# Kernel optimization log

Hardware: AMD Instinct MI355X
Metric: run time of the kernel (lower is better)

Reference implementation:

```python
import jax, jax.numpy as jnp
import numpy as np

N, I, O, ITERS = 65536, 16, 16, 3
EPS = 1e-8


def hamilton(q, r):
    # Hamilton quaternion product, broadcasting over leading dims; q, r: [..., 4]
    w1, x1, y1, z1 = jnp.moveaxis(q, -1, 0)
    w2, x2, y2, z2 = jnp.moveaxis(r, -1, 0)
    return jnp.stack([
        w1 * w2 - x1 * x2 - y1 * y2 - z1 * z2,
        w1 * x2 + x1 * w2 + y1 * z2 - z1 * y2,
        w1 * y2 - x1 * z2 + y1 * w2 + z1 * x2,
        w1 * z2 + x1 * y2 - y1 * x2 + z1 * w2,
    ], axis=-1)


def squash(s):
    # capsule squash nonlinearity along the last (quaternion) axis
    n2 = jnp.sum(s * s, axis=-1, keepdims=True)
    return s * (n2 / (1.0 + n2)) / jnp.sqrt(n2 + EPS)


def setup_inputs() -> dict:
    key = jax.random.key(0)
    ks = jax.random.split(key, 7)
    return {
        "x": jax.random.normal(ks[0], (N, I, 4), dtype=jnp.float32),
        "quats": jax.random.normal(ks[1], (O, I, 4), dtype=jnp.float32),
        "scale": jax.random.normal(ks[2], (O, I, 1), dtype=jnp.float32),
        "trans": jax.random.normal(ks[3], (O, I, 3), dtype=jnp.float32),
        "bias": jax.random.normal(ks[4], (O,), dtype=jnp.float32),
        "beta": jax.random.normal(ks[5], (O,), dtype=jnp.float32),
        "alpha": jax.random.normal(ks[6], (O,), dtype=jnp.float32),
    }


def reference(x, quats, scale, trans, bias, beta, alpha):
    # normalize learned quaternions to unit rotations: [O, I, 4]
    qn = quats / jnp.sqrt(jnp.sum(quats * quats, axis=-1, keepdims=True) + EPS)
    # votes: rotate each input capsule pose by each (out,in) quaternion -> [N, O, I, 4]
    votes = scale[None] * hamilton(qn[None], x[:, None])
    # translate the vector (imaginary) part of the vote quaternion
    votes = jnp.concatenate([votes[..., :1], votes[..., 1:] + trans[None]], axis=-1)

    b = jnp.zeros((x.shape[0], O, I), dtype=x.dtype)  # routing logits
    for _ in range(ITERS):
        c = jax.nn.softmax(b, axis=1)                    # couple over output caps
        s = jnp.einsum('noi,noid->nod', c, votes)        # weighted vote sum [N,O,4]
        v = squash(s)                                    # output poses [N,O,4]
        b = b + jnp.einsum('nod,noid->noi', v, votes)    # agreement update

    norm_s = jnp.sqrt(jnp.sum(s * s, axis=-1) + EPS)     # [N, O]
    a = jax.nn.sigmoid(beta * norm_s + alpha + bias)     # output activations [N, O]
    return v * a[..., None]                              # activation-scaled poses [N,O,4]
```

## Files before the change

### kernel.cpp

```cpp
#include <hip/hip_runtime.h>
#include <math.h>

#define EPSQ 1e-8f
#define LOG2E 1.4426950408889634f

typedef float f2 __attribute__((ext_vector_type(2)));

__device__ __forceinline__ float rcp_fast(float x) { return __builtin_amdgcn_rcpf(x); }
__device__ __forceinline__ float rsq_fast(float x) { return __builtin_amdgcn_rsqf(x); }
__device__ __forceinline__ f2 pk_fma(f2 a, f2 b, f2 c) { return __builtin_elementwise_fma(a, b, c); }

#define DPP_F(x, ctrl) \
    __int_as_float(__builtin_amdgcn_update_dpp(0, __float_as_int(x), (ctrl), 0xF, 0xF, true))

__device__ __forceinline__ float allsum16(float v) {
    v += DPP_F(v, 0xB1);
    v += DPP_F(v, 0x4E);
    v += DPP_F(v, 0x124);
    v += DPP_F(v, 0x128);
    return v;
}

__global__ __launch_bounds__(256, 4) void caps_kernel(
    const float* __restrict__ x,
    const float* __restrict__ quats,
    const float* __restrict__ scale,
    const float* __restrict__ trans,
    const float* __restrict__ bias,
    const float* __restrict__ beta,
    const float* __restrict__ alpha,
    float* __restrict__ out)
{
    __shared__ __align__(16) float qs[16][16][4];
    __shared__ __align__(16) float tr[16][16][4];
    __shared__ __align__(16) float xs[16][68];

    const int tid = threadIdx.x;
    const int o   = tid & 15;
    const int ln  = tid >> 4;

    {
        const int o2 = tid & 15, i2 = tid >> 4;
        const int pidx = o2 * 16 + i2;
        const float4 q = ((const float4*)quats)[pidx];
        const float sc = scale[pidx];
        const float qn2 = q.x*q.x + q.y*q.y + q.z*q.z + q.w*q.w;
        const float f = sc * rsq_fast(qn2 + EPSQ);
        qs[i2][o2][0] = q.x * f;
        qs[i2][o2][1] = q.y * f;
        qs[i2][o2][2] = q.z * f;
        qs[i2][o2][3] = q.w * f;
        tr[i2][o2][0] = 0.0f;
        tr[i2][o2][1] = trans[pidx*3 + 0];
        tr[i2][o2][2] = trans[pidx*3 + 1];
        tr[i2][o2][3] = trans[pidx*3 + 2];
    }
    {
        const float4 xv = ((const float4*)x)[(size_t)blockIdx.x * 256 + tid];
        *(float4*)&xs[tid >> 4][(tid & 15) * 4] = xv;
    }
    __syncthreads();

    f2 vwx[16], vyz[16];
    #pragma unroll
    for (int i = 0; i < 16; ++i) {
        const float4 q4 = *(const float4*)&qs[i][o][0];
        const float4 t4 = *(const float4*)&tr[i][o][0];
        const float4 x4 = *(const float4*)&xs[ln][i * 4];
        f2 a, b2;
        a = pk_fma(f2{ q4.x,  q4.x}, f2{x4.x, x4.y}, f2{t4.x, t4.y});
        a = pk_fma(f2{-q4.y,  q4.y}, f2{x4.y, x4.x}, a);
        a = pk_fma(f2{-q4.z,  q4.z}, f2{x4.z, x4.w}, a);
        a = pk_fma(f2{-q4.w, -q4.w}, f2{x4.w, x4.z}, a);
        b2 = pk_fma(f2{ q4.x,  q4.x}, f2{x4.z, x4.w}, f2{t4.z, t4.w});
        b2 = pk_fma(f2{-q4.y,  q4.y}, f2{x4.w, x4.z}, b2);
        b2 = pk_fma(f2{ q4.z, -q4.z}, f2{x4.x, x4.y}, b2);
        b2 = pk_fma(f2{ q4.w,  q4.w}, f2{x4.y, x4.x}, b2);
        vwx[i] = a; vyz[i] = b2;
    }

    f2 vl01, vl23;
    f2 v001, v023;
    f2 s01, s23, v01, v23;

    {
        f2 u01 = f2{0.f, 0.f}, u23 = f2{0.f, 0.f};
        #pragma unroll
        for (int i = 0; i < 16; ++i) { u01 += vwx[i]; u23 += vyz[i]; }
        f2 d = u01 * u01;
        d = pk_fma(u23, u23, d);
        const float n2 = (d.x + d.y) * (1.0f / 256.0f);
        const float f = n2 * rcp_fast(1.f + n2) * rsq_fast(n2 + EPSQ) * 0.0625f;
        v001 = u01 * f; v023 = u23 * f;
        vl01 = v001 * LOG2E; vl23 = v023 * LOG2E;
    }

    #pragma unroll
    for (int it = 1; it < 3; ++it) {
        f2 sn01 = f2{0.f, 0.f}, sn23 = f2{0.f, 0.f};
        #pragma unroll
        for (int i = 0; i < 16; ++i) {
            f2 d = vl01 * vwx[i];
            d = pk_fma(vl23, vyz[i], d);
            const float e  = __builtin_amdgcn_exp2f(d.x + d.y);
            const float se = allsum16(e);
            const float c  = e * rcp_fast(se);
            sn01 = pk_fma(f2{c, c}, vwx[i], sn01);
            sn23 = pk_fma(f2{c, c}, vyz[i], sn23);
        }
        s01 = sn01; s23 = sn23;
        const float n2 = s01.x*s01.x + s01.y*s01.y + s23.x*s23.x + s23.y*s23.y;
        const float f = n2 * rcp_fast(1.f + n2) * rsq_fast(n2 + EPSQ);
        v01 = s01 * f; v23 = s23 * f;
        if (it == 1) {
            vl01 = (v001 + v01) * LOG2E;
            vl23 = (v023 + v23) * LOG2E;
        }
    }

    const float n2f = s01.x*s01.x + s01.y*s01.y + s23.x*s23.x + s23.y*s23.y;
    const float norm_s = sqrtf(n2f + EPSQ);
    const float tgt = beta[o] * norm_s + alpha[o] + bias[o];
    const float a = rcp_fast(1.f + __builtin_amdgcn_exp2f(-tgt * LOG2E));
    float4 ov;
    ov.x = v01.x * a; ov.y = v01.y * a; ov.z = v23.x * a; ov.w = v23.y * a;
    ((float4*)out)[(size_t)blockIdx.x * 256 + tid] = ov;
}

extern "C" void kernel_launch(void* const* d_in, const int* in_sizes, int n_in,
                              void* d_out, int out_size, void* d_ws, size_t ws_size,
                              hipStream_t stream) {
    const float* x     = (const float*)d_in[0];
    const float* quats = (const float*)d_in[1];
    const float* scale = (const float*)d_in[2];
    const float* trans = (const float*)d_in[3];
    const float* bias  = (const float*)d_in[4];
    const float* beta  = (const float*)d_in[5];
    const float* alpha = (const float*)d_in[6];
    float* out = (float*)d_out;

    const int N = in_sizes[0] / 64;
    dim3 grid(N / 16), block(256);
    caps_kernel<<<grid, block, 0, stream>>>(x, quats, scale, trans, bias, beta, alpha, out);
}
```

Before: 97.56 us.

## Split input-capsule dimension across lanes and precompute weight table in setup kernel

Each thread now handles four input capsules instead of sixteen, with the per-sample reduction over inputs done via cross-row shuffles, and the grid grows to four samples per block. Quaternion normalization and sign-arranged coefficients are precomputed once by a separate one-block setup kernel into workspace, so the main kernel's prologue is plain copies. This aims to cut registers per thread and increase parallelism, at the cost of four times more blocks, redundant table loads per block, extra shuffle reductions, an extra launch, and only a quarter of lanes writing output.

```diff
diff --git a/kernel.cpp b/kernel.cpp
--- a/kernel.cpp
+++ b/kernel.cpp
@@ -20,111 +20,134 @@
     v += DPP_F(v, 0x128);
     return v;
 }
+__device__ __forceinline__ float allsum_rows(float v) {
+    v += __shfl_xor(v, 16);
+    v += __shfl_xor(v, 32);
+    return v;
+}
+
+__global__ void setup_kernel(const float* __restrict__ quats,
+                             const float* __restrict__ scale,
+                             const float* __restrict__ trans,
+                             float4* __restrict__ ws) {
+    const int t = threadIdx.x;
+    const int k = t >> 6, l = t & 63;
+    const int r = l >> 4, o = l & 15;
+    const int i = 4 * k + r;
+    const int pidx = o * 16 + i;
+    const float4 q = ((const float4*)quats)[pidx];
+    const float sc = scale[pidx];
+    const float f = sc * rsq_fast(q.x*q.x + q.y*q.y + q.z*q.z + q.w*q.w + EPSQ);
+    const float w = q.x * f, x = q.y * f, y = q.z * f, z = q.w * f;
+    ws[t]       = make_float4( w,  w, -x,  x);
+    ws[256 + t] = make_float4(-y,  y, -z, -z);
+    ws[512 + t] = make_float4(0.f, trans[pidx*3+0], trans[pidx*3+1], trans[pidx*3+2]);
+}
 
 __global__ __launch_bounds__(256, 4) void caps_kernel(
-    const float* __restrict__ x,
-    const float* __restrict__ quats,
-    const float* __restrict__ scale,
-    const float* __restrict__ trans,
-    const float* __restrict__ bias,
-    const float* __restrict__ beta,
-    const float* __restrict__ alpha,
+    const float*  __restrict__ x,
+    const float4* __restrict__ ws,
+    const float*  __restrict__ bias,
+    const float*  __restrict__ beta,
+    const float*  __restrict__ alpha,
     float* __restrict__ out)
 {
-    __shared__ __align__(16) float qs[16][16][4];
-    __shared__ __align__(16) float tr[16][16][4];
-    __shared__ __align__(16) float xs[16][68];
+    __shared__ __align__(16) float4 tabA[256];
+    __shared__ __align__(16) float4 tabB[256];
+    __shared__ __align__(16) float4 tabC[256];
+    __shared__ __align__(16) float4 xs[64];
+    __shared__ __align__(16) float4 xsw[64];
 
     const int tid = threadIdx.x;
-    const int o   = tid & 15;
-    const int ln  = tid >> 4;
-
-    {
-        const int o2 = tid & 15, i2 = tid >> 4;
-        const int pidx = o2 * 16 + i2;
-        const float4 q = ((const float4*)quats)[pidx];
-        const float sc = scale[pidx];
-        const float qn2 = q.x*q.x + q.y*q.y + q.z*q.z + q.w*q.w;
-        const float f = sc * rsq_fast(qn2 + EPSQ);
-        qs[i2][o2][0] = q.x * f;
-        qs[i2][o2][1] = q.y * f;
-        qs[i2][o2][2] = q.z * f;
-        qs[i2][o2][3] = q.w * f;
-        tr[i2][o2][0] = 0.0f;
-        tr[i2][o2][1] = trans[pidx*3 + 0];
-        tr[i2][o2][2] = trans[pidx*3 + 1];
-        tr[i2][o2][3] = trans[pidx*3 + 2];
-    }
-    {
-        const float4 xv = ((const float4*)x)[(size_t)blockIdx.x * 256 + tid];
-        *(float4*)&xs[tid >> 4][(tid & 15) * 4] = xv;
+    tabA[tid] = ws[tid];
+    tabB[tid] = ws[256 + tid];
+    tabC[tid] = ws[512 + tid];
+    if (tid < 64) {
+        const float4 xv = ((const float4*)x)[(size_t)blockIdx.x * 64 + tid];
+        xs[tid]  = xv;
+        xsw[tid] = make_float4(xv.y, xv.x, xv.w, xv.z);
     }
     __syncthreads();
 
-    f2 vwx[16], vyz[16];
+    const int w = tid >> 6;
+    const int l = tid & 63;
+    const int r = l >> 4;
+    const int o = l & 15;
+
+    f2 vwx[4], vyz[4];
     #pragma unroll
-    for (int i = 0; i < 16; ++i) {
-        const float4 q4 = *(const float4*)&qs[i][o][0];
-        const float4 t4 = *(const float4*)&tr[i][o][0];
-        const float4 x4 = *(const float4*)&xs[ln][i * 4];
-        f2 a, b2;
-        a = pk_fma(f2{ q4.x,  q4.x}, f2{x4.x, x4.y}, f2{t4.x, t4.y});
-        a = pk_fma(f2{-q4.y,  q4.y}, f2{x4.y, x4.x}, a);
-        a = pk_fma(f2{-q4.z,  q4.z}, f2{x4.z, x4.w}, a);
-        a = pk_fma(f2{-q4.w, -q4.w}, f2{x4.w, x4.z}, a);
-        b2 = pk_fma(f2{ q4.x,  q4.x}, f2{x4.z, x4.w}, f2{t4.z, t4.w});
-        b2 = pk_fma(f2{-q4.y,  q4.y}, f2{x4.w, x4.z}, b2);
-        b2 = pk_fma(f2{ q4.z, -q4.z}, f2{x4.x, x4.y}, b2);
-        b2 = pk_fma(f2{ q4.w,  q4.w}, f2{x4.y, x4.x}, b2);
-        vwx[i] = a; vyz[i] = b2;
+    for (int k = 0; k < 4; ++k) {
+        const int rec = k * 64 + l;
+        const float4 A = tabA[rec];
+        const float4 B = tabB[rec];
+        const float4 C = tabC[rec];
+        const int xi = w * 16 + 4 * k + r;
+        const float4 xv = xs[xi];
+        const float4 xw = xsw[xi];
+        const f2 m0  = f2{A.x, A.y}, m1  = f2{A.z, A.w};
+        const f2 m2  = f2{B.x, B.y}, m3  = f2{B.z, B.w};
+        const f2 P0  = f2{xv.x, xv.y}, P1  = f2{xv.z, xv.w};
+        const f2 P0s = f2{xw.x, xw.y}, P1s = f2{xw.z, xw.w};
+        f2 a = pk_fma(m0, P0, f2{C.x, C.y});
+        a = pk_fma(m1, P0s, a);
+        a = pk_fma(m2, P1,  a);
+        a = pk_fma(m3, P1s, a);
+        f2 b2 = pk_fma(m0, P1, f2{C.z, C.w});
+        b2 = pk_fma(m1, P1s, b2);
+        b2 = pk_fma(-m2, P0,  b2);
+        b2 = pk_fma(-m3, P0s, b2);
+        vwx[k] = a; vyz[k] = b2;
     }
 
-    f2 vl01, vl23;
-    f2 v001, v023;
-    f2 s01, s23, v01, v23;
-
+    f2 v0wx, v0yz, vlwx, vlyz;
     {
-        f2 u01 = f2{0.f, 0.f}, u23 = f2{0.f, 0.f};
-        #pragma unroll
-        for (int i = 0; i < 16; ++i) { u01 += vwx[i]; u23 += vyz[i]; }
-        f2 d = u01 * u01;
-        d = pk_fma(u23, u23, d);
+        f2 uwx = (vwx[0] + vwx[1]) + (vwx[2] + vwx[3]);
+        f2 uyz = (vyz[0] + vyz[1]) + (vyz[2] + vyz[3]);
+        uwx.x = allsum_rows(uwx.x); uwx.y = allsum_rows(uwx.y);
+        uyz.x = allsum_rows(uyz.x); uyz.y = allsum_rows(uyz.y);
+        f2 d = uwx * uwx; d = pk_fma(uyz, uyz, d);
         const float n2 = (d.x + d.y) * (1.0f / 256.0f);
-        const float f = n2 * rcp_fast(1.f + n2) * rsq_fast(n2 + EPSQ) * 0.0625f;
-        v001 = u01 * f; v023 = u23 * f;
-        vl01 = v001 * LOG2E; vl23 = v023 * LOG2E;
+        const float fq = n2 * rcp_fast(1.f + n2) * rsq_fast(n2 + EPSQ) * 0.0625f;
+        v0wx = uwx * fq; v0yz = uyz * fq;
+        vlwx = v0wx * LOG2E; vlyz = v0yz * LOG2E;
     }
 
+    f2 s_wx, s_yz, vowx, voyz;
     #pragma unroll
     for (int it = 1; it < 3; ++it) {
-        f2 sn01 = f2{0.f, 0.f}, sn23 = f2{0.f, 0.f};
+        f2 snwx = f2{0.f, 0.f}, snyz = f2{0.f, 0.f};
         #pragma unroll
-        for (int i = 0; i < 16; ++i) {
-            f2 d = vl01 * vwx[i];
-            d = pk_fma(vl23, vyz[i], d);
-            const float e  = __builtin_amdgcn_exp2f(d.x + d.y);
+        for (int k = 0; k < 4; ++k) {
+            f2 d2 = vlwx * vwx[k];
+            d2 = pk_fma(vlyz, vyz[k], d2);
+            const float e  = __builtin_amdgcn_exp2f(d2.x + d2.y);
             const float se = allsum16(e);
             const float c  = e * rcp_fast(se);
-            sn01 = pk_fma(f2{c, c}, vwx[i], sn01);
-            sn23 = pk_fma(f2{c, c}, vyz[i], sn23);
+            snwx = pk_fma(f2{c, c}, vwx[k], snwx);
+            snyz = pk_fma(f2{c, c}, vyz[k], snyz);
         }
-        s01 = sn01; s23 = sn23;
-        const float n2 = s01.x*s01.x + s01.y*s01.y + s23.x*s23.x + s23.y*s23.y;
-        const float f = n2 * rcp_fast(1.f + n2) * rsq_fast(n2 + EPSQ);
-        v01 = s01 * f; v23 = s23 * f;
+        snwx.x = allsum_rows(snwx.x); snwx.y = allsum_rows(snwx.y);
+        snyz.x = allsum_rows(snyz.x); snyz.y = allsum_rows(snyz.y);
+        const float n2 = snwx.x*snwx.x + snwx.y*snwx.y + snyz.x*snyz.x + snyz.y*snyz.y;
+        const float fq = n2 * rcp_fast(1.f + n2) * rsq_fast(n2 + EPSQ);
+        vowx = snwx * fq; voyz = snyz * fq;
+        s_wx = snwx; s_yz = snyz;
         if (it == 1) {
-            vl01 = (v001 + v01) * LOG2E;
-            vl23 = (v023 + v23) * LOG2E;
+            vlwx = (v0wx + vowx) * LOG2E;
+            vlyz = (v0yz + voyz) * LOG2E;
         }
     }
 
-    const float n2f = s01.x*s01.x + s01.y*s01.y + s23.x*s23.x + s23.y*s23.y;
+    const float n2f = s_wx.x*s_wx.x + s_wx.y*s_wx.y + s_yz.x*s_yz.x + s_yz.y*s_yz.y;
     const float norm_s = sqrtf(n2f + EPSQ);
     const float tgt = beta[o] * norm_s + alpha[o] + bias[o];
-    const float a = rcp_fast(1.f + __builtin_amdgcn_exp2f(-tgt * LOG2E));
-    float4 ov;
-    ov.x = v01.x * a; ov.y = v01.y * a; ov.z = v23.x * a; ov.w = v23.y * a;
-    ((float4*)out)[(size_t)blockIdx.x * 256 + tid] = ov;
+    const float aAct = rcp_fast(1.f + __builtin_amdgcn_exp2f(-tgt * LOG2E));
+    if (r == 0) {
+        float4 ov;
+        ov.x = vowx.x * aAct; ov.y = vowx.y * aAct;
+        ov.z = voyz.x * aAct; ov.w = voyz.y * aAct;
+        ((float4*)out)[((size_t)blockIdx.x * 4 + w) * 16 + o] = ov;
+    }
 }
 
 extern "C" void kernel_launch(void* const* d_in, const int* in_sizes, int n_in,
@@ -138,8 +161,9 @@
     const float* beta  = (const float*)d_in[5];
     const float* alpha = (const float*)d_in[6];
     float* out = (float*)d_out;
+    float4* wsv = (float4*)d_ws;
 
     const int N = in_sizes[0] / 64;
-    dim3 grid(N / 16), block(256);
-    caps_kernel<<<grid, block, 0, stream>>>(x, quats, scale, trans, bias, beta, alpha, out);
+    setup_kernel<<<1, 256, 0, stream>>>(quats, scale, trans, wsv);
+    caps_kernel<<<N / 4, 256, 0, stream>>>(x, wsv, bias, beta, alpha, out);
 }
```

Result: slower. 108.9 us (+11.7%).

## Process four tiles per block with double-buffered x prefetch

Applied to the files above, without the earlier changes.

Each block now handles four 16-sample tiles, strided by the grid size, instead of one. The per-block setup (normalising the quaternions, loading the translations, and loading beta/alpha/bias) is amortised across those tiles. The next tile's x is loaded from global memory into registers before the current tile's routing is computed, then written to a second shared buffer. The grid shrinks by 4x, which reduces the number of waves in flight and the latency hiding that came from many small blocks.

```diff
diff --git a/kernel.cpp b/kernel.cpp
--- a/kernel.cpp
+++ b/kernel.cpp
@@ -3,6 +3,7 @@
 
 #define EPSQ 1e-8f
 #define LOG2E 1.4426950408889634f
+#define TILES_PER_BLOCK 4
 
 typedef float f2 __attribute__((ext_vector_type(2)));
 
@@ -29,11 +30,12 @@
     const float* __restrict__ bias,
     const float* __restrict__ beta,
     const float* __restrict__ alpha,
-    float* __restrict__ out)
+    float* __restrict__ out,
+    int tiles_total)
 {
     __shared__ __align__(16) float qs[16][16][4];
     __shared__ __align__(16) float tr[16][16][4];
-    __shared__ __align__(16) float xs[16][68];
+    __shared__ __align__(16) float xs[2][16][68];
 
     const int tid = threadIdx.x;
     const int o   = tid & 15;
@@ -55,76 +57,96 @@
         tr[i2][o2][2] = trans[pidx*3 + 1];
         tr[i2][o2][3] = trans[pidx*3 + 2];
     }
+    const float beta_o = beta[o];
+    const float ab_o   = alpha[o] + bias[o];
+
+    size_t tile = blockIdx.x;
     {
-        const float4 xv = ((const float4*)x)[(size_t)blockIdx.x * 256 + tid];
-        *(float4*)&xs[tid >> 4][(tid & 15) * 4] = xv;
+        const float4 xv = ((const float4*)x)[tile * 256 + tid];
+        *(float4*)&xs[0][tid >> 4][(tid & 15) * 4] = xv;
     }
     __syncthreads();
 
-    f2 vwx[16], vyz[16];
     #pragma unroll
-    for (int i = 0; i < 16; ++i) {
-        const float4 q4 = *(const float4*)&qs[i][o][0];
-        const float4 t4 = *(const float4*)&tr[i][o][0];
-        const float4 x4 = *(const float4*)&xs[ln][i * 4];
-        f2 a, b2;
-        a = pk_fma(f2{ q4.x,  q4.x}, f2{x4.x, x4.y}, f2{t4.x, t4.y});
-        a = pk_fma(f2{-q4.y,  q4.y}, f2{x4.y, x4.x}, a);
-        a = pk_fma(f2{-q4.z,  q4.z}, f2{x4.z, x4.w}, a);
-        a = pk_fma(f2{-q4.w, -q4.w}, f2{x4.w, x4.z}, a);
-        b2 = pk_fma(f2{ q4.x,  q4.x}, f2{x4.z, x4.w}, f2{t4.z, t4.w});
-        b2 = pk_fma(f2{-q4.y,  q4.y}, f2{x4.w, x4.z}, b2);
-        b2 = pk_fma(f2{ q4.z, -q4.z}, f2{x4.x, x4.y}, b2);
-        b2 = pk_fma(f2{ q4.w,  q4.w}, f2{x4.y, x4.x}, b2);
-        vwx[i] = a; vyz[i] = b2;
-    }
+    for (int t = 0; t < TILES_PER_BLOCK; ++t) {
+        float4 xnext;
+        const size_t ntile = tile + gridDim.x;
+        if (t < TILES_PER_BLOCK - 1)
+            xnext = ((const float4*)x)[ntile * 256 + tid];
 
-    f2 vl01, vl23;
-    f2 v001, v023;
-    f2 s01, s23, v01, v23;
+        const int buf = t & 1;
 
-    {
-        f2 u01 = f2{0.f, 0.f}, u23 = f2{0.f, 0.f};
-        #pragma unroll
-        for (int i = 0; i < 16; ++i) { u01 += vwx[i]; u23 += vyz[i]; }
-        f2 d = u01 * u01;
-        d = pk_fma(u23, u23, d);
-        const float n2 = (d.x + d.y) * (1.0f / 256.0f);
-        const float f = n2 * rcp_fast(1.f + n2) * rsq_fast(n2 + EPSQ) * 0.0625f;
-        v001 = u01 * f; v023 = u23 * f;
-        vl01 = v001 * LOG2E; vl23 = v023 * LOG2E;
-    }
-
-    #pragma unroll
-    for (int it = 1; it < 3; ++it) {
-        f2 sn01 = f2{0.f, 0.f}, sn23 = f2{0.f, 0.f};
+        f2 vwx[16], vyz[16];
         #pragma unroll
         for (int i = 0; i < 16; ++i) {
-            f2 d = vl01 * vwx[i];
-            d = pk_fma(vl23, vyz[i], d);
-            const float e  = __builtin_amdgcn_exp2f(d.x + d.y);
-            const float se = allsum16(e);
-            const float c  = e * rcp_fast(se);
-            sn01 = pk_fma(f2{c, c}, vwx[i], sn01);
-            sn23 = pk_fma(f2{c, c}, vyz[i], sn23);
+            const float4 q4 = *(const float4*)&qs[i][o][0];
+            const float4 t4 = *(const float4*)&tr[i][o][0];
+            const float4 x4 = *(const float4*)&xs[buf][ln][i * 4];
+            f2 a, b2;
+            a = pk_fma(f2{ q4.x,  q4.x}, f2{x4.x, x4.y}, f2{t4.x, t4.y});
+            a = pk_fma(f2{-q4.y,  q4.y}, f2{x4.y, x4.x}, a);
+            a = pk_fma(f2{-q4.z,  q4.z}, f2{x4.z, x4.w}, a);
+            a = pk_fma(f2{-q4.w, -q4.w}, f2{x4.w, x4.z}, a);
+            b2 = pk_fma(f2{ q4.x,  q4.x}, f2{x4.z, x4.w}, f2{t4.z, t4.w});
+            b2 = pk_fma(f2{-q4.y,  q4.y}, f2{x4.w, x4.z}, b2);
+            b2 = pk_fma(f2{ q4.z, -q4.z}, f2{x4.x, x4.y}, b2);
+            b2 = pk_fma(f2{ q4.w,  q4.w}, f2{x4.y, x4.x}, b2);
+            vwx[i] = a; vyz[i] = b2;
         }
-        s01 = sn01; s23 = sn23;
-        const float n2 = s01.x*s01.x + s01.y*s01.y + s23.x*s23.x + s23.y*s23.y;
-        const float f = n2 * rcp_fast(1.f + n2) * rsq_fast(n2 + EPSQ);
-        v01 = s01 * f; v23 = s23 * f;
-        if (it == 1) {
-            vl01 = (v001 + v01) * LOG2E;
-            vl23 = (v023 + v23) * LOG2E;
+
+        f2 vlwx, vlyz, v0wx, v0yz;
+
+        {
+            f2 uwx = f2{0.f, 0.f}, uyz = f2{0.f, 0.f};
+            #pragma unroll
+            for (int i = 0; i < 16; ++i) { uwx += vwx[i]; uyz += vyz[i]; }
+            f2 d = uwx * uwx;
+            d = pk_fma(uyz, uyz, d);
+            const float n2 = (d.x + d.y) * (1.0f / 256.0f);
+            const float fq = n2 * rcp_fast(1.f + n2) * rsq_fast(n2 + EPSQ) * 0.0625f;
+            v0wx = uwx * fq; v0yz = uyz * fq;
+            vlwx = v0wx * LOG2E; vlyz = v0yz * LOG2E;
+        }
+
+        f2 s_wx, s_yz, vowx, voyz;
+        #pragma unroll
+        for (int it = 1; it < 3; ++it) {
+            f2 snwx = f2{0.f, 0.f}, snyz = f2{0.f, 0.f};
+            #pragma unroll
+            for (int i = 0; i < 16; ++i) {
+                f2 d2 = vlwx * vwx[i];
+                d2 = pk_fma(vlyz, vyz[i], d2);
+                const float e  = __builtin_amdgcn_exp2f(d2.x + d2.y);
+                const float se = allsum16(e);
+                const float c  = e * rcp_fast(se);
+                snwx = pk_fma(f2{c, c}, vwx[i], snwx);
+                snyz = pk_fma(f2{c, c}, vyz[i], snyz);
+            }
+            s_wx = snwx; s_yz = snyz;
+            const float n2 = snwx.x*snwx.x + snwx.y*snwx.y + snyz.x*snyz.x + snyz.y*snyz.y;
+            const float fq = n2 * rcp_fast(1.f + n2) * rsq_fast(n2 + EPSQ);
+            vowx = snwx * fq; voyz = snyz * fq;
+            if (it == 1) {
+                vlwx = (v0wx + vowx) * LOG2E;
+                vlyz = (v0yz + voyz) * LOG2E;
+            }
+        }
+
+        const float n2f = s_wx.x*s_wx.x + s_wx.y*s_wx.y + s_yz.x*s_yz.x + s_yz.y*s_yz.y;
+        const float norm_s = sqrtf(n2f + EPSQ);
+        const float tgt = beta_o * norm_s + ab_o;
+        const float aAct = rcp_fast(1.f + __builtin_amdgcn_exp2f(-tgt * LOG2E));
+        float4 ov;
+        ov.x = vowx.x * aAct; ov.y = vowx.y * aAct;
+        ov.z = voyz.x * aAct; ov.w = voyz.y * aAct;
+        ((float4*)out)[tile * 256 + tid] = ov;
+
+        if (t < TILES_PER_BLOCK - 1) {
+            *(float4*)&xs[buf ^ 1][tid >> 4][(tid & 15) * 4] = xnext;
+            __syncthreads();
+            tile = ntile;
         }
     }
-
-    const float n2f = s01.x*s01.x + s01.y*s01.y + s23.x*s23.x + s23.y*s23.y;
-    const float norm_s = sqrtf(n2f + EPSQ);
-    const float tgt = beta[o] * norm_s + alpha[o] + bias[o];
-    const float a = rcp_fast(1.f + __builtin_amdgcn_exp2f(-tgt * LOG2E));
-    float4 ov;
-    ov.x = v01.x * a; ov.y = v01.y * a; ov.z = v23.x * a; ov.w = v23.y * a;
-    ((float4*)out)[(size_t)blockIdx.x * 256 + tid] = ov;
 }
 
 extern "C" void kernel_launch(void* const* d_in, const int* in_sizes, int n_in,
@@ -140,6 +162,8 @@
     float* out = (float*)d_out;
 
     const int N = in_sizes[0] / 64;
-    dim3 grid(N / 16), block(256);
-    caps_kernel<<<grid, block, 0, stream>>>(x, quats, scale, trans, bias, beta, alpha, out);
+    const int tiles = N / 16;
+    const int grid = tiles / TILES_PER_BLOCK;
+    caps_kernel<<<grid, 256, 0, stream>>>(x, quats, scale, trans, bias, beta, alpha,
+                                          out, tiles);
 }
```

Result: no change. 99.22 us (+1.7%).
